# Kernel tuning notes

Measured on AMD Instinct MI355X. Metric: run time of the kernel, lower is better.

## Reference

```python
import jax, jax.numpy as jnp
import numpy as np

INPUT = 28
HID = 64
OUT = 10


def setup_inputs() -> dict:
    key = jax.random.key(0)
    ks = jax.random.split(key, 8)
    s_ih = 1.0 / np.sqrt(HID)
    x = jax.random.normal(ks[0], (16384, 28, INPUT), dtype=jnp.float32)
    # PyTorch LSTM params: gate order (i, f, g, o), each block of size HID
    W_ih = jax.random.uniform(ks[1], (4 * HID, INPUT), jnp.float32, -s_ih, s_ih)
    W_hh = jax.random.uniform(ks[2], (4 * HID, HID), jnp.float32, -s_ih, s_ih)
    b_ih = jax.random.uniform(ks[3], (4 * HID,), jnp.float32, -s_ih, s_ih)
    b_hh = jax.random.uniform(ks[4], (4 * HID,), jnp.float32, -s_ih, s_ih)
    s_fc = 1.0 / np.sqrt(HID)
    W_fc = jax.random.uniform(ks[5], (OUT, HID), jnp.float32, -s_fc, s_fc)
    b_fc = jax.random.uniform(ks[6], (OUT,), jnp.float32, -s_fc, s_fc)
    return {"x": x, "W_ih": W_ih, "W_hh": W_hh, "b_ih": b_ih, "b_hh": b_hh,
            "W_fc": W_fc, "b_fc": b_fc}


def reference(x, W_ih, W_hh, b_ih, b_hh, W_fc, b_fc):
    B = x.shape[0]
    # Precompute input projections for all timesteps in one big GEMM: [T, B, 4H]
    x_proj = jnp.einsum('bti,gi->tbg', x, W_ih) + (b_ih + b_hh)

    def step(carry, xp_t):
        h, c = carry
        gates = xp_t + h @ W_hh.T  # [B, 4H]
        i, f, g, o = jnp.split(gates, 4, axis=-1)
        i = jax.nn.sigmoid(i)
        f = jax.nn.sigmoid(f)
        g = jnp.tanh(g)
        o = jax.nn.sigmoid(o)
        c = f * c + i * g
        h = o * jnp.tanh(c)
        return (h, c), None

    h0 = jnp.zeros((B, HID), dtype=x.dtype)
    c0 = jnp.zeros((B, HID), dtype=x.dtype)
    (h_last, _), _ = jax.lax.scan(step, (h0, c0), x_proj)
    # fc on the last timestep's hidden state (== output[:, -1, :])
    return h_last @ W_fc.T + b_fc
```

## Files before the change

kernel.cpp:

```cpp
#include <hip/hip_runtime.h>
#include <hip/hip_bf16.h>


namespace {
constexpr int B_TOT   = 16384;
constexpr int T_STEPS = 28;
constexpr int IN_DIM  = 28;
constexpr int HID     = 64;
constexpr int OUT_DIM = 10;
constexpr int ROWS    = 16;
constexpr int THREADS = 256;
constexpr int KP      = 104;
constexpr int XROW    = T_STEPS * IN_DIM;
constexpr int NFRAG   = 16 * 3;
constexpr int WS_ELEMS = NFRAG * 64 * 8;
}

typedef __attribute__((ext_vector_type(8))) short short8v;
typedef __attribute__((ext_vector_type(4))) short short4v;
typedef __attribute__((ext_vector_type(4))) float float4v;

__device__ __forceinline__ short f2bf_cold(float f) {
  union { float f; unsigned u; } v; v.f = f;
  unsigned r = v.u + 0x7FFFu + ((v.u >> 16) & 1u);
  return (short)(r >> 16);
}
__device__ __forceinline__ float bf2f(short s) {
  union { unsigned u; float f; } v; v.u = ((unsigned)(unsigned short)s) << 16;
  return v.f;
}
__device__ __forceinline__ unsigned pk2(float a, float b) {
  __hip_bfloat162 h = __float22bfloat162_rn(float2{a, b});
  union { __hip_bfloat162 h; unsigned u; } cv; cv.h = h; return cv.u;
}

__global__ void lstm_prep(const float* __restrict__ W_ih,
                          const float* __restrict__ W_hh,
                          const float* __restrict__ b_ih,
                          const float* __restrict__ b_hh,
                          unsigned short* __restrict__ ws) {
  int idx = blockIdx.x * blockDim.x + threadIdx.x;
  if (idx >= WS_ELEMS) return;
  int j  = idx & 7;
  int l  = (idx >> 3) & 63;
  int fk = idx >> 9;
  int kc = fk % 3;
  int mt = fk / 3;
  int m  = 16 * mt + (l & 15);
  int unit = m >> 2, type = m & 3;
  int g  = type * 64 + unit;
  int k  = kc * 32 + (l >> 4) * 8 + j;
  float v = 0.0f;
  if (k < IN_DIM)        v = W_ih[g * IN_DIM + k];
  else if (k == IN_DIM)  v = b_ih[g] + b_hh[g];
  else if (k >= 32)      v = W_hh[g * HID + (k - 32)];
  ws[idx] = (unsigned short)f2bf_cold(v);
}

__global__ __attribute__((amdgpu_flat_work_group_size(THREADS, THREADS),
                          amdgpu_waves_per_eu(4, 4)))
void lstm_mfma8(const float* __restrict__ x,
                const unsigned short* __restrict__ wfrag,
                const float* __restrict__ W_fc,
                const float* __restrict__ b_fc, float* __restrict__ out) {
  __shared__ short hs[2][ROWS][KP];

  const int tid  = threadIdx.x;
  const int lane = tid & 63;
  const int w    = tid >> 6;
  const int l15  = lane & 15;
  const int q    = lane >> 4;
  const int b0   = blockIdx.x * ROWS;

  short8v a[4][3];
#pragma unroll
  for (int i = 0; i < 4; ++i)
#pragma unroll
    for (int kc = 0; kc < 3; ++kc)
      a[i][kc] = *(const short8v*)&wfrag[((((4 * w + i) * 3) + kc) * 64 + lane) * 8];

  for (int idx = tid; idx < 2 * ROWS * KP; idx += THREADS) (&hs[0][0][0])[idx] = 0;
  __syncthreads();
  if (tid < 2 * ROWS) hs[tid >> 4][tid & 15][IN_DIM] = (short)0x3F80;

  const bool stager = (lane < 28);
  const int  s  = w * 28 + lane;
  const int  sr = s / 7;
  const int  sc = s - 7 * sr;
  const float* xptr = x + (size_t)(b0 + sr) * XROW + sc * 4;

  float4 xfly = {0.f, 0.f, 0.f, 0.f};
  if (stager) {
    float4 x0 = *(const float4*)xptr;
    short4v sv;
    unsigned plo = pk2(x0.x, x0.y), phi = pk2(x0.z, x0.w);
    sv[0] = (short)(plo & 0xFFFF); sv[1] = (short)(plo >> 16);
    sv[2] = (short)(phi & 0xFFFF); sv[3] = (short)(phi >> 16);
    *(short4v*)&hs[0][sr][sc * 4] = sv;
    xfly = *(const float4*)(xptr + 1 * IN_DIM);
  }
  __syncthreads();

  float c_state[4] = {0.f, 0.f, 0.f, 0.f};

  for (int t = 0; t < T_STEPS; ++t) {
    const int cur = t & 1, nxt = cur ^ 1;

    short8v bf0 = *(const short8v*)&hs[cur][l15][q * 8];
    short8v bf1 = *(const short8v*)&hs[cur][l15][32 + q * 8];
    short8v bf2 = *(const short8v*)&hs[cur][l15][64 + q * 8];

    if (stager) {
      if (t + 1 < T_STEPS) {
        short4v sv;
        unsigned plo = pk2(xfly.x, xfly.y), phi = pk2(xfly.z, xfly.w);
        sv[0] = (short)(plo & 0xFFFF); sv[1] = (short)(plo >> 16);
        sv[2] = (short)(phi & 0xFFFF); sv[3] = (short)(phi >> 16);
        *(short4v*)&hs[nxt][sr][sc * 4] = sv;
      }
      if (t + 2 < T_STEPS)
        xfly = *(const float4*)(xptr + (t + 2) * IN_DIM);
    }

    const float4v zero4 = {0.f, 0.f, 0.f, 0.f};
    float4v acc[4];
#pragma unroll
    for (int i = 0; i < 4; ++i)
      acc[i] = __builtin_amdgcn_mfma_f32_16x16x32_bf16(a[i][0], bf0, zero4, 0, 0, 0);
#pragma unroll
    for (int i = 0; i < 4; ++i)
      acc[i] = __builtin_amdgcn_mfma_f32_16x16x32_bf16(a[i][1], bf1, acc[i], 0, 0, 0);
#pragma unroll
    for (int i = 0; i < 4; ++i)
      acc[i] = __builtin_amdgcn_mfma_f32_16x16x32_bf16(a[i][2], bf2, acc[i], 0, 0, 0);

    float hv[4];
#pragma unroll
    for (int i = 0; i < 4; ++i) {
      float4v g4 = acc[i];
      float Ei = __expf(-g4[0]);
      float Ef = __expf(-g4[1]);
      float Eg = __expf(-2.0f * g4[2]);
      float Eo = __expf(-g4[3]);
      float di = 1.0f + Ei, df = 1.0f + Ef;
      float r1 = __builtin_amdgcn_rcpf(di * df);
      float iv = r1 * df;
      float fv = r1 * di;
      float gv = fmaf(2.0f, __builtin_amdgcn_rcpf(1.0f + Eg), -1.0f);
      float cn = fmaf(fv, c_state[i], iv * gv);
      c_state[i] = cn;
      float ct = fminf(fmaxf(cn, -15.0f), 15.0f);
      float Ec = __expf(-2.0f * ct);
      float dn = 1.0f + Eo, dc = 1.0f + Ec;
      float r2 = __builtin_amdgcn_rcpf(dn * dc);
      float ov = r2 * dc;
      float tc = fmaf(2.0f * r2, dn, -1.0f);
      hv[i] = ov * tc;
    }
    unsigned p01 = pk2(hv[0], hv[1]);
    unsigned p23 = pk2(hv[2], hv[3]);
    hs[nxt][l15][32 + 16 * w + 0 + q]  = (short)(p01 & 0xFFFF);
    hs[nxt][l15][32 + 16 * w + 4 + q]  = (short)(p01 >> 16);
    hs[nxt][l15][32 + 16 * w + 8 + q]  = (short)(p23 & 0xFFFF);
    hs[nxt][l15][32 + 16 * w + 12 + q] = (short)(p23 >> 16);

    __syncthreads();
  }

  if (tid < ROWS * OUT_DIM) {
    const int r = tid / OUT_DIM;
    const int o = tid - r * OUT_DIM;
    float sacc = b_fc[o];
#pragma unroll
    for (int j = 0; j < HID; ++j)
      sacc += bf2f(hs[0][r][32 + j]) * W_fc[o * HID + j];
    out[(b0 + r) * OUT_DIM + o] = sacc;
  }
}

extern "C" void kernel_launch(void* const* d_in, const int* in_sizes, int n_in,
                              void* d_out, int out_size, void* d_ws, size_t ws_size,
                              hipStream_t stream) {
  const float* x    = (const float*)d_in[0];
  const float* W_ih = (const float*)d_in[1];
  const float* W_hh = (const float*)d_in[2];
  const float* b_ih = (const float*)d_in[3];
  const float* b_hh = (const float*)d_in[4];
  const float* W_fc = (const float*)d_in[5];
  const float* b_fc = (const float*)d_in[6];
  float* out = (float*)d_out;
  unsigned short* ws = (unsigned short*)d_ws;

  lstm_prep<<<(WS_ELEMS + 255) / 256, 256, 0, stream>>>(W_ih, W_hh, b_ih, b_hh, ws);

  dim3 grid(B_TOT / ROWS);
  dim3 block(THREADS);
  lstm_mfma8<<<grid, block, 0, stream>>>(x, ws, W_fc, b_fc, out);
}
```

Baseline: 132.7 us.

## Split LSTM gate tiles across 8 waves, fold exp2 scaling into weights, pack h stores

Doubles the block to 512 threads so each wave owns 2 gate M-tiles instead of 4. That halves the serial MFMA and activation chain each wave runs per timestep, at the cost of a larger barrier. The prep kernel pre-scales weights by -log2(e) (or -2·log2(e) for the g gate), so raw exp2 replaces expf with negation. Hidden-unit columns are permuted so each lane writes its two h values as one 32-bit LDS store, and the FC weight indexing is remapped to match. Prescaling before bf16 rounding slightly changes numerics.

```diff
diff --git a/kernel.cpp b/kernel.cpp
--- a/kernel.cpp
+++ b/kernel.cpp
@@ -9,7 +9,7 @@
 constexpr int HID     = 64;
 constexpr int OUT_DIM = 10;
 constexpr int ROWS    = 16;
-constexpr int THREADS = 256;
+constexpr int THREADS = 512;
 constexpr int KP      = 104;
 constexpr int XROW    = T_STEPS * IN_DIM;
 constexpr int NFRAG   = 16 * 3;
@@ -53,12 +53,17 @@
   float v = 0.0f;
   if (k < IN_DIM)        v = W_ih[g * IN_DIM + k];
   else if (k == IN_DIM)  v = b_ih[g] + b_hh[g];
-  else if (k >= 32)      v = W_hh[g * HID + (k - 32)];
+  else if (k >= 32) {
+    int c = k - 32;
+    int u = 8 * (c >> 3) + 4 * (c & 1) + ((c >> 1) & 3);
+    v = W_hh[g * HID + u];
+  }
+  v *= (type == 2) ? -2.8853900817779268f : -1.4426950408889634f;
   ws[idx] = (unsigned short)f2bf_cold(v);
 }
 
 __global__ __attribute__((amdgpu_flat_work_group_size(THREADS, THREADS),
-                          amdgpu_waves_per_eu(4, 4)))
+                          amdgpu_waves_per_eu(8, 8)))
 void lstm_mfma8(const float* __restrict__ x,
                 const unsigned short* __restrict__ wfrag,
                 const float* __restrict__ W_fc,
@@ -72,19 +77,19 @@
   const int q    = lane >> 4;
   const int b0   = blockIdx.x * ROWS;
 
-  short8v a[4][3];
-#pragma unroll
-  for (int i = 0; i < 4; ++i)
+  short8v a[2][3];
+#pragma unroll
+  for (int i = 0; i < 2; ++i)
 #pragma unroll
     for (int kc = 0; kc < 3; ++kc)
-      a[i][kc] = *(const short8v*)&wfrag[((((4 * w + i) * 3) + kc) * 64 + lane) * 8];
+      a[i][kc] = *(const short8v*)&wfrag[((((2 * w + i) * 3) + kc) * 64 + lane) * 8];
 
   for (int idx = tid; idx < 2 * ROWS * KP; idx += THREADS) (&hs[0][0][0])[idx] = 0;
   __syncthreads();
   if (tid < 2 * ROWS) hs[tid >> 4][tid & 15][IN_DIM] = (short)0x3F80;
 
-  const bool stager = (lane < 28);
-  const int  s  = w * 28 + lane;
+  const bool stager = (lane < 14);
+  const int  s  = w * 14 + lane;
   const int  sr = s / 7;
   const int  sc = s - 7 * sr;
   const float* xptr = x + (size_t)(b0 + sr) * XROW + sc * 4;
@@ -101,7 +106,7 @@
   }
   __syncthreads();
 
-  float c_state[4] = {0.f, 0.f, 0.f, 0.f};
+  float c_state[2] = {0.f, 0.f};
 
   for (int t = 0; t < T_STEPS; ++t) {
     const int cur = t & 1, nxt = cur ^ 1;
@@ -123,25 +128,25 @@
     }
 
     const float4v zero4 = {0.f, 0.f, 0.f, 0.f};
-    float4v acc[4];
-#pragma unroll
-    for (int i = 0; i < 4; ++i)
+    float4v acc[2];
+#pragma unroll
+    for (int i = 0; i < 2; ++i)
       acc[i] = __builtin_amdgcn_mfma_f32_16x16x32_bf16(a[i][0], bf0, zero4, 0, 0, 0);
 #pragma unroll
-    for (int i = 0; i < 4; ++i)
+    for (int i = 0; i < 2; ++i)
       acc[i] = __builtin_amdgcn_mfma_f32_16x16x32_bf16(a[i][1], bf1, acc[i], 0, 0, 0);
 #pragma unroll
-    for (int i = 0; i < 4; ++i)
+    for (int i = 0; i < 2; ++i)
       acc[i] = __builtin_amdgcn_mfma_f32_16x16x32_bf16(a[i][2], bf2, acc[i], 0, 0, 0);
 
-    float hv[4];
-#pragma unroll
-    for (int i = 0; i < 4; ++i) {
+    float hv[2];
+#pragma unroll
+    for (int i = 0; i < 2; ++i) {
       float4v g4 = acc[i];
-      float Ei = __expf(-g4[0]);
-      float Ef = __expf(-g4[1]);
-      float Eg = __expf(-2.0f * g4[2]);
-      float Eo = __expf(-g4[3]);
+      float Ei = __builtin_amdgcn_exp2f(g4[0]);
+      float Ef = __builtin_amdgcn_exp2f(g4[1]);
+      float Eg = __builtin_amdgcn_exp2f(g4[2]);
+      float Eo = __builtin_amdgcn_exp2f(g4[3]);
       float di = 1.0f + Ei, df = 1.0f + Ef;
       float r1 = __builtin_amdgcn_rcpf(di * df);
       float iv = r1 * df;
@@ -150,7 +155,7 @@
       float cn = fmaf(fv, c_state[i], iv * gv);
       c_state[i] = cn;
       float ct = fminf(fmaxf(cn, -15.0f), 15.0f);
-      float Ec = __expf(-2.0f * ct);
+      float Ec = __builtin_amdgcn_exp2f(-2.8853900817779268f * ct);
       float dn = 1.0f + Eo, dc = 1.0f + Ec;
       float r2 = __builtin_amdgcn_rcpf(dn * dc);
       float ov = r2 * dc;
@@ -158,11 +163,7 @@
       hv[i] = ov * tc;
     }
     unsigned p01 = pk2(hv[0], hv[1]);
-    unsigned p23 = pk2(hv[2], hv[3]);
-    hs[nxt][l15][32 + 16 * w + 0 + q]  = (short)(p01 & 0xFFFF);
-    hs[nxt][l15][32 + 16 * w + 4 + q]  = (short)(p01 >> 16);
-    hs[nxt][l15][32 + 16 * w + 8 + q]  = (short)(p23 & 0xFFFF);
-    hs[nxt][l15][32 + 16 * w + 12 + q] = (short)(p23 >> 16);
+    *(unsigned*)&hs[nxt][l15][32 + 8 * w + 2 * q] = p01;
 
     __syncthreads();
   }
@@ -172,8 +173,10 @@
     const int o = tid - r * OUT_DIM;
     float sacc = b_fc[o];
 #pragma unroll
-    for (int j = 0; j < HID; ++j)
-      sacc += bf2f(hs[0][r][32 + j]) * W_fc[o * HID + j];
+    for (int c = 0; c < HID; ++c) {
+      int u = 8 * (c >> 3) + 4 * (c & 1) + ((c >> 1) & 3);
+      sacc += bf2f(hs[0][r][32 + c]) * W_fc[o * HID + u];
+    }
     out[(b0 + r) * OUT_DIM + o] = sacc;
   }
 }
```

Measured after the change: 133.1 us. No clear change (+0.3%).
